# Optimization experiments

Measured on AMD Instinct MI355X. Metric: run time of the kernel, lower is better.

## Reference

```python
import jax, jax.numpy as jnp
import numpy as np

N_ROWS = 8192
EMBED_DIM = 256


def setup_inputs() -> dict:
    key = jax.random.key(0)
    k1, k2, k3, k4, k5 = jax.random.split(key, 5)
    M = jax.random.normal(k1, (N_ROWS, EMBED_DIM), dtype=jnp.float32)
    N = jax.random.normal(k2, (N_ROWS, EMBED_DIM), dtype=jnp.float32)
    # gate_w: nn.Linear(embed_dim, 1) -> weight [1, d], bias [1]; gate_b extra scalar param [1]
    Wg = jax.random.normal(k3, (1, EMBED_DIM), dtype=jnp.float32) * 0.06
    bg = jax.random.normal(k4, (1,), dtype=jnp.float32) * 0.1
    gate_b = jax.random.normal(k5, (1,), dtype=jnp.float32) * 0.1
    return {"M": M, "N": N, "Wg": Wg, "bg": bg, "gate_b": gate_b, "iseval": 0}


def reference(M, N, Wg, bg, gate_b, iseval):
    # mt: [n, n] cross-similarity scores
    mt = jnp.matmul(N, M.T)
    if not iseval:
        # training branch: zero out the diagonal (mt - diag(diag(mt)))
        n = mt.shape[0]
        idx = jnp.arange(n)
        mt = mt.at[idx, idx].set(0.0)
    else:
        # eval branch: zero out the first row
        mt = mt.at[0].set(0.0)
    attn_weight = jax.nn.softmax(mt, axis=-1)          # [n, n]
    out_attn = jnp.matmul(attn_weight, M)              # [n, d]
    gate = jax.nn.sigmoid(jnp.matmul(out_attn, Wg.T) + bg + gate_b)  # [n, 1]
    boosted = out_attn * gate + N * (1.0 - gate)       # [n, d]
    return boosted[:, None, None, :]                   # [n, 1, 1, d]
```

## Files before the change

### kernel.cpp

```cpp
#include <hip/hip_runtime.h>


constexpr int EMBED = 256;
constexpr int BQ = 64;
constexpr int BJ = 32;
constexpr int NT = 256;

constexpr int SS_OFF = 0;
constexpr int SS_BUF = 18432;
constexpr int PH_OFF = 36864;
constexpr int PH_BUF = 5120;
constexpr int AS_OFF = 47104;
constexpr int AS_BUF = 256;
constexpr int LDS_SZ = 47616;

typedef _Float16 half8 __attribute__((ext_vector_type(8)));
typedef float f32x4 __attribute__((ext_vector_type(4)));
typedef short short8v __attribute__((ext_vector_type(8)));

static __device__ __forceinline__ f32x4 mfma16(half8 a, half8 b, f32x4 c) {
    return __builtin_amdgcn_mfma_f32_16x16x32_f16(a, b, c, 0, 0, 0);
}
static __device__ __forceinline__ short f2h(float x) {
    return (short)__builtin_bit_cast(unsigned short, (_Float16)x);
}

__global__ void prep(const float* __restrict__ M,
                     short* __restrict__ MhG, short* __restrict__ MtG) {
    __shared__ float L[16 * 260];
    const int r0 = blockIdx.x * 16;
    const int t = threadIdx.x;
    const int pj = t >> 4, pc = (t & 15) * 16;
    {
        const float* src = M + (size_t)(r0 + pj) * EMBED + pc;
        float4 v[4];
        #pragma unroll
        for (int i = 0; i < 4; ++i) v[i] = ((const float4*)src)[i];
        short* hd = MhG + (size_t)(r0 + pj) * EMBED + pc;
        #pragma unroll
        for (int i = 0; i < 2; ++i) {
            float4 a = v[2 * i], b = v[2 * i + 1];
            short8v h;
            h[0]=f2h(a.x); h[1]=f2h(a.y); h[2]=f2h(a.z); h[3]=f2h(a.w);
            h[4]=f2h(b.x); h[5]=f2h(b.y); h[6]=f2h(b.z); h[7]=f2h(b.w);
            *(short8v*)(hd + 8 * i) = h;
        }
        #pragma unroll
        for (int i = 0; i < 4; ++i)
            *(float4*)(L + pj * 260 + pc + 4 * i) = v[i];
    }
    __syncthreads();
    {
        const int d = t;
        const int tile = r0 >> 5, jh = (r0 >> 4) & 1;
        short* dst = MtG + (size_t)tile * (BJ * EMBED) + d * BJ + jh * 16;
        #pragma unroll
        for (int g2 = 0; g2 < 2; ++g2) {
            short8v w;
            #pragma unroll
            for (int e = 0; e < 8; ++e) w[e] = f2h(L[(g2 * 8 + e) * 260 + d]);
            *(short8v*)(dst + g2 * 8) = w;
        }
    }
}

__launch_bounds__(NT, 2)
__global__ void attn(const short* __restrict__ MhG, const short* __restrict__ MtG,
                     const float* __restrict__ Ng, const int* __restrict__ iseval_p,
                     float* __restrict__ O0out, short* __restrict__ Ofp,
                     float* __restrict__ MLm, float* __restrict__ MLl, int n)
{
    __shared__ __align__(16) char smem[LDS_SZ];

    const int t = threadIdx.x, lane = t & 63, wave = t >> 6;
    const int quad = lane >> 4, mn = lane & 15;
    const int bid = blockIdx.x;
    const int s  = (bid & 7) >> 1;
    const int qb = ((bid >> 3) << 1) | (bid & 1);
    const int q0 = qb * BQ;
    const int jbase = s * (n >> 2);
    const int jb32 = jbase / BJ;
    const int ntiles = (n >> 2) / BJ;
    const int iseval = *iseval_p;
    const int jt = wave & 1, kh = wave >> 1;
    const int dq = wave;
    const int sq = t >> 2, sh = t & 3;

    const float L2E = 1.4426950408889634f;
    half8 Qf[4][4];
    #pragma unroll
    for (int qi = 0; qi < 4; ++qi) {
        const float* np = Ng + (size_t)(q0 + qi * 16 + mn) * EMBED;
        #pragma unroll
        for (int kk = 0; kk < 4; ++kk) {
            const float* p = np + (kh * 4 + kk) * 32 + quad * 8;
            float4 a = *(const float4*)p, b = *(const float4*)(p + 4);
            half8 h;
            h[0]=(_Float16)(a.x*L2E); h[1]=(_Float16)(a.y*L2E);
            h[2]=(_Float16)(a.z*L2E); h[3]=(_Float16)(a.w*L2E);
            h[4]=(_Float16)(b.x*L2E); h[5]=(_Float16)(b.y*L2E);
            h[6]=(_Float16)(b.z*L2E); h[7]=(_Float16)(b.w*L2E);
            Qf[qi][kk] = h;
        }
    }

    f32x4 O[4][4];
    #pragma unroll
    for (int qi = 0; qi < 4; ++qi)
        #pragma unroll
        for (int dt = 0; dt < 4; ++dt) O[qi][dt] = (f32x4){0.f, 0.f, 0.f, 0.f};

    float m_reg = -1e30f, l_reg = 0.f;

    const short* mhb0 = MhG + (size_t)(jbase + jt * 16 + mn) * EMBED + kh * 128 + quad * 8;
    half8 Bc[4], Bn[4], Mtf[4];
    #pragma unroll
    for (int kk = 0; kk < 4; ++kk) Bc[kk] = *(const half8*)(mhb0 + kk * 32);

    __syncthreads();

    for (int tt = 0; tt <= ntiles; ++tt) {
        const int bw = tt & 1;
        const int br = bw ^ 1;

        if (tt > 0) {
            const short* mtb = MtG + (size_t)(jb32 + (tt - 1)) * (BJ * EMBED);
            #pragma unroll
            for (int dt = 0; dt < 4; ++dt)
                Mtf[dt] = *(const half8*)(mtb + (dq * 64 + dt * 16 + mn) * BJ + quad * 8);
        }

        if (tt < ntiles) {
            f32x4 a0 = (f32x4){0,0,0,0}, a1 = (f32x4){0,0,0,0};
            f32x4 a2 = (f32x4){0,0,0,0}, a3 = (f32x4){0,0,0,0};
            #pragma unroll
            for (int kk = 0; kk < 4; ++kk) {
                half8 bf = Bc[kk];
                a0 = mfma16(Qf[0][kk], bf, a0);
                a1 = mfma16(Qf[1][kk], bf, a1);
                a2 = mfma16(Qf[2][kk], bf, a2);
                a3 = mfma16(Qf[3][kk], bf, a3);
            }
            float* ssp = (float*)(smem + SS_OFF + bw * SS_BUF) + kh * 2304;
            #pragma unroll
            for (int r = 0; r < 4; ++r) {
                ssp[(0  + quad * 4 + r) * 36 + jt * 16 + mn] = a0[r];
                ssp[(16 + quad * 4 + r) * 36 + jt * 16 + mn] = a1[r];
                ssp[(32 + quad * 4 + r) * 36 + jt * 16 + mn] = a2[r];
                ssp[(48 + quad * 4 + r) * 36 + jt * 16 + mn] = a3[r];
            }
        }

        if (tt + 1 < ntiles) {
            const short* nb = mhb0 + (size_t)(tt + 1) * (BJ * EMBED);
            #pragma unroll
            for (int kk = 0; kk < 4; ++kk) Bn[kk] = *(const half8*)(nb + kk * 32);
        }

        if (tt > 0) {
            const int j0g = jbase + (tt - 1) * BJ;
            const float* p0 = (const float*)(smem + SS_OFF + br * SS_BUF) + sq * 36 + 8 * sh;
            float4 sa = *(const float4*)p0;
            float4 sb = *(const float4*)(p0 + 4);
            float4 sc = *(const float4*)(p0 + 2304);
            float4 sd = *(const float4*)(p0 + 2308);
            float sv[8] = {sa.x + sc.x, sa.y + sc.y, sa.z + sc.z, sa.w + sc.w,
                           sb.x + sd.x, sb.y + sd.y, sb.z + sd.z, sb.w + sd.w};
            const int qg = q0 + sq;
            if (iseval) {
                if (qg == 0) {
                    #pragma unroll
                    for (int i = 0; i < 8; ++i) sv[i] = 0.f;
                }
            } else {
                int dj = qg - j0g - 8 * sh;
                #pragma unroll
                for (int i = 0; i < 8; ++i) if (dj == i) sv[i] = 0.f;
            }
            float mx = sv[0];
            #pragma unroll
            for (int i = 1; i < 8; ++i) mx = fmaxf(mx, sv[i]);
            mx = fmaxf(mx, __shfl_xor(mx, 1));
            mx = fmaxf(mx, __shfl_xor(mx, 2));
            float m_new = fmaxf(m_reg, mx);
            float alpha = exp2f(m_reg - m_new);
            float p[8], ps = 0.f;
            #pragma unroll
            for (int i = 0; i < 8; ++i) { p[i] = exp2f(sv[i] - m_new); ps += p[i]; }
            ps += __shfl_xor(ps, 1);
            ps += __shfl_xor(ps, 2);
            m_reg = m_new;
            l_reg = l_reg * alpha + ps;
            if (sh == 0)
                ((float*)(smem + AS_OFF + br * AS_BUF))[sq] = alpha;
            half8 ph;
            #pragma unroll
            for (int i = 0; i < 8; ++i) ph[i] = (_Float16)p[i];
            *(half8*)(smem + PH_OFF + br * PH_BUF + sq * 80 + sh * 16) = ph;
        }

        __syncthreads();

        if (tt > 0) {
            #pragma unroll
            for (int qi = 0; qi < 4; ++qi) {
                half8 pf = *(const half8*)(smem + PH_OFF + br * PH_BUF + (qi * 16 + mn) * 80 + quad * 16);
                f32x4 al = *(const f32x4*)((const float*)(smem + AS_OFF + br * AS_BUF) + qi * 16 + quad * 4);
                #pragma unroll
                for (int dt = 0; dt < 4; ++dt) {
                    f32x4 o = O[qi][dt];
                    o[0] *= al[0]; o[1] *= al[1]; o[2] *= al[2]; o[3] *= al[3];
                    O[qi][dt] = mfma16(pf, Mtf[dt], o);
                }
            }
        }

        #pragma unroll
        for (int kk = 0; kk < 4; ++kk) Bc[kk] = Bn[kk];
    }

    if (s == 0) {
        #pragma unroll
        for (int qi = 0; qi < 4; ++qi)
            #pragma unroll
            for (int dt = 0; dt < 4; ++dt) {
                int col = dq * 64 + dt * 16 + mn;
                #pragma unroll
                for (int r = 0; r < 4; ++r)
                    O0out[(size_t)(q0 + qi * 16 + quad * 4 + r) * EMBED + col] = O[qi][dt][r];
            }
    } else {
        short* dst = Ofp + (size_t)(s - 1) * n * EMBED;
        #pragma unroll
        for (int qi = 0; qi < 4; ++qi)
            #pragma unroll
            for (int dt = 0; dt < 4; ++dt) {
                int col = dq * 64 + dt * 16 + mn;
                #pragma unroll
                for (int r = 0; r < 4; ++r)
                    dst[(size_t)(q0 + qi * 16 + quad * 4 + r) * EMBED + col] = f2h(O[qi][dt][r]);
            }
    }
    if (sh == 0) {
        MLm[s * n + q0 + sq] = m_reg;
        MLl[s * n + q0 + sq] = l_reg;
    }
}

__global__ void combine4(const float* __restrict__ O0, const short* __restrict__ Ofp,
                         const float* __restrict__ MLm, const float* __restrict__ MLl,
                         const float* __restrict__ Ng, const float* __restrict__ Wg,
                         const float* __restrict__ bg, const float* __restrict__ gb,
                         float* __restrict__ out, int n)
{
    const int t = threadIdx.x;
    const int row = blockIdx.x * 16 + (t >> 4);
    const int c = t & 15;
    float ms[4], ls[4];
    #pragma unroll
    for (int k = 0; k < 4; ++k) { ms[k] = MLm[k * n + row]; ls[k] = MLl[k * n + row]; }
    float m = fmaxf(fmaxf(ms[0], ms[1]), fmaxf(ms[2], ms[3]));
    float w[4], lsum = 0.f;
    #pragma unroll
    for (int k = 0; k < 4; ++k) { w[k] = exp2f(ms[k] - m); lsum += w[k] * ls[k]; }
    float linv = 1.f / lsum;

    float acc[16];
    {
        const float4* o0 = (const float4*)(O0 + (size_t)row * EMBED + c * 16);
        #pragma unroll
        for (int i = 0; i < 4; ++i) {
            float4 v = o0[i];
            acc[4*i+0] = w[0] * v.x; acc[4*i+1] = w[0] * v.y;
            acc[4*i+2] = w[0] * v.z; acc[4*i+3] = w[0] * v.w;
        }
    }
    #pragma unroll
    for (int k = 1; k < 4; ++k) {
        const short* op = Ofp + (size_t)(k - 1) * n * EMBED + (size_t)row * EMBED + c * 16;
        half8 a = *(const half8*)op, b = *(const half8*)(op + 8);
        #pragma unroll
        for (int i = 0; i < 8; ++i) {
            acc[i]     += w[k] * (float)a[i];
            acc[8 + i] += w[k] * (float)b[i];
        }
    }
    float dot = 0.f;
    #pragma unroll
    for (int i = 0; i < 16; ++i) { acc[i] *= linv; dot += acc[i] * Wg[c * 16 + i]; }
    dot += __shfl_xor(dot, 1);
    dot += __shfl_xor(dot, 2);
    dot += __shfl_xor(dot, 4);
    dot += __shfl_xor(dot, 8);
    float g = 1.f / (1.f + __expf(-(dot + bg[0] + gb[0])));
    const float4* n4 = (const float4*)(Ng + (size_t)row * EMBED + c * 16);
    float4* o4 = (float4*)(out + (size_t)row * EMBED + c * 16);
    #pragma unroll
    for (int i = 0; i < 4; ++i) {
        float4 nn = n4[i];
        float4 res;
        res.x = acc[4*i+0] * g + nn.x * (1.f - g);
        res.y = acc[4*i+1] * g + nn.y * (1.f - g);
        res.z = acc[4*i+2] * g + nn.z * (1.f - g);
        res.w = acc[4*i+3] * g + nn.w * (1.f - g);
        o4[i] = res;
    }
}

extern "C" void kernel_launch(void* const* d_in, const int* in_sizes, int n_in,
                              void* d_out, int out_size, void* d_ws, size_t ws_size,
                              hipStream_t stream) {
    const float* M      = (const float*)d_in[0];
    const float* N      = (const float*)d_in[1];
    const float* Wgp    = (const float*)d_in[2];
    const float* bgp    = (const float*)d_in[3];
    const float* gbp    = (const float*)d_in[4];
    const int*   iseval = (const int*)d_in[5];
    float* out = (float*)d_out;

    int n = in_sizes[0] / EMBED;
    short* MhG = (short*)d_ws;
    short* MtG = MhG + (size_t)n * EMBED;
    short* Ofp = MtG + (size_t)n * EMBED;
    float* MLm = (float*)(Ofp + (size_t)3 * n * EMBED);
    float* MLl = MLm + 4 * n;

    hipLaunchKernelGGL(prep, dim3(n / 16), dim3(NT), 0, stream, M, MhG, MtG);
    hipLaunchKernelGGL(attn, dim3((n / BQ) * 4), dim3(NT), 0, stream,
                       MhG, MtG, N, iseval, out, Ofp, MLm, MLl, n);
    hipLaunchKernelGGL(combine4, dim3(n / 16), dim3(NT), 0, stream,
                       out, Ofp, MLm, MLl, N, Wgp, bgp, gbp, out, n);
}
```

Measured before the change: 185.0 us.

## Widen key tile to 64 and drop skewed double-buffered pipeline

Doubles the key-tile width from 32 to 64, so each block runs half as many loop iterations and barrier pairs per key range. Each thread now handles 16 scores per row in the online softmax, and the P·V step issues two MFMAs per output fragment using two 32-key chunks of the transposed M. The previous one-tile-skewed schedule with double-buffered LDS scores and probabilities is replaced by a single buffer with two barriers per iteration. This saves LDS and loop overhead, but the QK^T of the next tile no longer overlaps the softmax and PV of the current tile, and the extra fragment arrays raise register use.

```diff
diff --git a/kernel.cpp b/kernel.cpp
--- a/kernel.cpp
+++ b/kernel.cpp
@@ -3,16 +3,14 @@
 
 constexpr int EMBED = 256;
 constexpr int BQ = 64;
-constexpr int BJ = 32;
+constexpr int BJ = 64;
 constexpr int NT = 256;
 
 constexpr int SS_OFF = 0;
-constexpr int SS_BUF = 18432;
-constexpr int PH_OFF = 36864;
-constexpr int PH_BUF = 5120;
-constexpr int AS_OFF = 47104;
-constexpr int AS_BUF = 256;
-constexpr int LDS_SZ = 47616;
+constexpr int SS_PLW = 4352;
+constexpr int PH_OFF = 34816;
+constexpr int AS_OFF = 44032;
+constexpr int LDS_SZ = 44288;
 
 typedef _Float16 half8 __attribute__((ext_vector_type(8)));
 typedef float f32x4 __attribute__((ext_vector_type(4)));
@@ -53,7 +51,7 @@
     {
         const int d = t;
         const int tile = r0 >> 5, jh = (r0 >> 4) & 1;
-        short* dst = MtG + (size_t)tile * (BJ * EMBED) + d * BJ + jh * 16;
+        short* dst = MtG + (size_t)tile * (32 * EMBED) + d * 32 + jh * 16;
         #pragma unroll
         for (int g2 = 0; g2 < 2; ++g2) {
             short8v w;
@@ -79,7 +77,7 @@
     const int qb = ((bid >> 3) << 1) | (bid & 1);
     const int q0 = qb * BQ;
     const int jbase = s * (n >> 2);
-    const int jb32 = jbase / BJ;
+    const int jb32 = jbase / 32;
     const int ntiles = (n >> 2) / BJ;
     const int iseval = *iseval_p;
     const int jt = wave & 1, kh = wave >> 1;
@@ -112,111 +110,125 @@
 
     float m_reg = -1e30f, l_reg = 0.f;
 
-    const short* mhb0 = MhG + (size_t)(jbase + jt * 16 + mn) * EMBED + kh * 128 + quad * 8;
-    half8 Bc[4], Bn[4], Mtf[4];
-    #pragma unroll
-    for (int kk = 0; kk < 4; ++kk) Bc[kk] = *(const half8*)(mhb0 + kk * 32);
-
-    __syncthreads();
-
-    for (int tt = 0; tt <= ntiles; ++tt) {
-        const int bw = tt & 1;
-        const int br = bw ^ 1;
-
-        if (tt > 0) {
-            const short* mtb = MtG + (size_t)(jb32 + (tt - 1)) * (BJ * EMBED);
+    const short* mhb0 = MhG + (size_t)(jbase + jt * 32 + mn) * EMBED + kh * 128 + quad * 8;
+    half8 Bc[2][4], Mtf[2][4];
+    #pragma unroll
+    for (int jtt = 0; jtt < 2; ++jtt)
+        #pragma unroll
+        for (int kk = 0; kk < 4; ++kk)
+            Bc[jtt][kk] = *(const half8*)(mhb0 + (size_t)jtt * 16 * EMBED + kk * 32);
+
+    for (int tt = 0; tt < ntiles; ++tt) {
+        #pragma unroll
+        for (int c = 0; c < 2; ++c) {
+            const short* mtb = MtG + (size_t)(jb32 + 2 * tt + c) * (32 * EMBED);
             #pragma unroll
             for (int dt = 0; dt < 4; ++dt)
-                Mtf[dt] = *(const half8*)(mtb + (dq * 64 + dt * 16 + mn) * BJ + quad * 8);
-        }
-
-        if (tt < ntiles) {
-            f32x4 a0 = (f32x4){0,0,0,0}, a1 = (f32x4){0,0,0,0};
-            f32x4 a2 = (f32x4){0,0,0,0}, a3 = (f32x4){0,0,0,0};
+                Mtf[c][dt] = *(const half8*)(mtb + (dq * 64 + dt * 16 + mn) * 32 + quad * 8);
+        }
+
+        {
+            f32x4 a[4][2];
+            #pragma unroll
+            for (int qi = 0; qi < 4; ++qi)
+                #pragma unroll
+                for (int jtt = 0; jtt < 2; ++jtt) a[qi][jtt] = (f32x4){0,0,0,0};
             #pragma unroll
             for (int kk = 0; kk < 4; ++kk) {
-                half8 bf = Bc[kk];
-                a0 = mfma16(Qf[0][kk], bf, a0);
-                a1 = mfma16(Qf[1][kk], bf, a1);
-                a2 = mfma16(Qf[2][kk], bf, a2);
-                a3 = mfma16(Qf[3][kk], bf, a3);
-            }
-            float* ssp = (float*)(smem + SS_OFF + bw * SS_BUF) + kh * 2304;
-            #pragma unroll
-            for (int r = 0; r < 4; ++r) {
-                ssp[(0  + quad * 4 + r) * 36 + jt * 16 + mn] = a0[r];
-                ssp[(16 + quad * 4 + r) * 36 + jt * 16 + mn] = a1[r];
-                ssp[(32 + quad * 4 + r) * 36 + jt * 16 + mn] = a2[r];
-                ssp[(48 + quad * 4 + r) * 36 + jt * 16 + mn] = a3[r];
-            }
+                #pragma unroll
+                for (int jtt = 0; jtt < 2; ++jtt) {
+                    half8 bf = Bc[jtt][kk];
+                    a[0][jtt] = mfma16(Qf[0][kk], bf, a[0][jtt]);
+                    a[1][jtt] = mfma16(Qf[1][kk], bf, a[1][jtt]);
+                    a[2][jtt] = mfma16(Qf[2][kk], bf, a[2][jtt]);
+                    a[3][jtt] = mfma16(Qf[3][kk], bf, a[3][jtt]);
+                }
+            }
+            float* ssp = (float*)(smem + SS_OFF) + kh * SS_PLW;
+            #pragma unroll
+            for (int qi = 0; qi < 4; ++qi)
+                #pragma unroll
+                for (int jtt = 0; jtt < 2; ++jtt)
+                    #pragma unroll
+                    for (int r = 0; r < 4; ++r)
+                        ssp[(qi * 16 + quad * 4 + r) * 68 + jt * 32 + jtt * 16 + mn] = a[qi][jtt][r];
         }
 
         if (tt + 1 < ntiles) {
             const short* nb = mhb0 + (size_t)(tt + 1) * (BJ * EMBED);
             #pragma unroll
-            for (int kk = 0; kk < 4; ++kk) Bn[kk] = *(const half8*)(nb + kk * 32);
-        }
-
-        if (tt > 0) {
-            const int j0g = jbase + (tt - 1) * BJ;
-            const float* p0 = (const float*)(smem + SS_OFF + br * SS_BUF) + sq * 36 + 8 * sh;
-            float4 sa = *(const float4*)p0;
-            float4 sb = *(const float4*)(p0 + 4);
-            float4 sc = *(const float4*)(p0 + 2304);
-            float4 sd = *(const float4*)(p0 + 2308);
-            float sv[8] = {sa.x + sc.x, sa.y + sc.y, sa.z + sc.z, sa.w + sc.w,
-                           sb.x + sd.x, sb.y + sd.y, sb.z + sd.z, sb.w + sd.w};
+            for (int jtt = 0; jtt < 2; ++jtt)
+                #pragma unroll
+                for (int kk = 0; kk < 4; ++kk)
+                    Bc[jtt][kk] = *(const half8*)(nb + (size_t)jtt * 16 * EMBED + kk * 32);
+        }
+
+        __syncthreads();
+
+        {
+            const int j0g = jbase + tt * BJ;
+            const float* p0 = (const float*)(smem + SS_OFF) + sq * 68 + 16 * sh;
+            float sv[16];
+            #pragma unroll
+            for (int g = 0; g < 4; ++g) {
+                float4 x = *(const float4*)(p0 + 4 * g);
+                float4 y = *(const float4*)(p0 + SS_PLW + 4 * g);
+                sv[4*g+0] = x.x + y.x; sv[4*g+1] = x.y + y.y;
+                sv[4*g+2] = x.z + y.z; sv[4*g+3] = x.w + y.w;
+            }
             const int qg = q0 + sq;
             if (iseval) {
                 if (qg == 0) {
                     #pragma unroll
-                    for (int i = 0; i < 8; ++i) sv[i] = 0.f;
+                    for (int i = 0; i < 16; ++i) sv[i] = 0.f;
                 }
             } else {
-                int dj = qg - j0g - 8 * sh;
-                #pragma unroll
-                for (int i = 0; i < 8; ++i) if (dj == i) sv[i] = 0.f;
+                int dj = qg - j0g - 16 * sh;
+                #pragma unroll
+                for (int i = 0; i < 16; ++i) if (dj == i) sv[i] = 0.f;
             }
             float mx = sv[0];
             #pragma unroll
-            for (int i = 1; i < 8; ++i) mx = fmaxf(mx, sv[i]);
+            for (int i = 1; i < 16; ++i) mx = fmaxf(mx, sv[i]);
             mx = fmaxf(mx, __shfl_xor(mx, 1));
             mx = fmaxf(mx, __shfl_xor(mx, 2));
             float m_new = fmaxf(m_reg, mx);
             float alpha = exp2f(m_reg - m_new);
-            float p[8], ps = 0.f;
-            #pragma unroll
-            for (int i = 0; i < 8; ++i) { p[i] = exp2f(sv[i] - m_new); ps += p[i]; }
+            float p[16], ps = 0.f;
+            #pragma unroll
+            for (int i = 0; i < 16; ++i) { p[i] = exp2f(sv[i] - m_new); ps += p[i]; }
             ps += __shfl_xor(ps, 1);
             ps += __shfl_xor(ps, 2);
             m_reg = m_new;
             l_reg = l_reg * alpha + ps;
             if (sh == 0)
-                ((float*)(smem + AS_OFF + br * AS_BUF))[sq] = alpha;
-            half8 ph;
-            #pragma unroll
-            for (int i = 0; i < 8; ++i) ph[i] = (_Float16)p[i];
-            *(half8*)(smem + PH_OFF + br * PH_BUF + sq * 80 + sh * 16) = ph;
+                ((float*)(smem + AS_OFF))[sq] = alpha;
+            char* pb = smem + PH_OFF + sq * 144 + sh * 32;
+            #pragma unroll
+            for (int g = 0; g < 2; ++g) {
+                half8 ph;
+                #pragma unroll
+                for (int i = 0; i < 8; ++i) ph[i] = (_Float16)p[8 * g + i];
+                *(half8*)(pb + 16 * g) = ph;
+            }
         }
 
         __syncthreads();
 
-        if (tt > 0) {
-            #pragma unroll
-            for (int qi = 0; qi < 4; ++qi) {
-                half8 pf = *(const half8*)(smem + PH_OFF + br * PH_BUF + (qi * 16 + mn) * 80 + quad * 16);
-                f32x4 al = *(const f32x4*)((const float*)(smem + AS_OFF + br * AS_BUF) + qi * 16 + quad * 4);
-                #pragma unroll
-                for (int dt = 0; dt < 4; ++dt) {
-                    f32x4 o = O[qi][dt];
-                    o[0] *= al[0]; o[1] *= al[1]; o[2] *= al[2]; o[3] *= al[3];
-                    O[qi][dt] = mfma16(pf, Mtf[dt], o);
-                }
-            }
-        }
-
-        #pragma unroll
-        for (int kk = 0; kk < 4; ++kk) Bc[kk] = Bn[kk];
+        #pragma unroll
+        for (int qi = 0; qi < 4; ++qi) {
+            const char* pr = smem + PH_OFF + (qi * 16 + mn) * 144 + quad * 16;
+            half8 pf0 = *(const half8*)pr;
+            half8 pf1 = *(const half8*)(pr + 64);
+            f32x4 al = *(const f32x4*)((const float*)(smem + AS_OFF) + qi * 16 + quad * 4);
+            #pragma unroll
+            for (int dt = 0; dt < 4; ++dt) {
+                f32x4 o = O[qi][dt];
+                o[0] *= al[0]; o[1] *= al[1]; o[2] *= al[2]; o[3] *= al[3];
+                o = mfma16(pf0, Mtf[0][dt], o);
+                O[qi][dt] = mfma16(pf1, Mtf[1][dt], o);
+            }
+        }
     }
 
     if (s == 0) {
```

Result: no change. 186.8 us (+0.9%).
